# Kernel tuning notes

Measured on AMD Instinct MI355X. Metric: run time of the kernel, lower is better.

The kernel has to match this reference:

```python
import jax, jax.numpy as jnp
import numpy as np

VOCAB = 50257
EMBED_DIM = 768


def setup_inputs() -> dict:
    key = jax.random.key(0)
    k1, k2 = jax.random.split(key)
    x = jax.random.randint(k1, (8, 2048), 0, VOCAB, dtype=jnp.int64 if jax.config.jax_enable_x64 else jnp.int32)
    weight = jax.random.normal(k2, (EMBED_DIM, VOCAB), dtype=jnp.float32)
    return {"x": x, "weight": weight}


def reference(x, weight):
    # Original: one_hot(x, vocab) @ weight.T  ==  gather rows of weight.T
    # weight: [embed_dim, vocab]; output: [batch, seq, embed_dim]
    return jnp.take(weight.T, x, axis=0)
```

## Files before the change

kernel.cpp:

```cpp
#include <hip/hip_runtime.h>


#define VOCAB 50257
#define EMBED 768
#define WINB 32
#define NWIN 1571
#define RG 8
#define ROWS 96
#define LSTRIDE 36
#define CAP 64

__device__ __forceinline__ int xcd_swizzle(int bid, int nwg) {
  const int NX = 8;
  int q = nwg / NX;
  int xcd = bid % NX, idx = bid / NX;
  return xcd * q + idx;
}

__global__ __launch_bounds__(256) void scatter_kernel(const int* __restrict__ x,
                                                      int* __restrict__ cur,
                                                      int* __restrict__ buckets,
                                                      int* __restrict__ spill_cnt,
                                                      int* __restrict__ spill,
                                                      int n) {
  int i = blockIdx.x * blockDim.x + threadIdx.x;
  if (i < n) {
    int v = x[i];
    int win = v >> 5;
    int p = atomicAdd(&cur[win], 1);
    if (p < CAP) {
      buckets[win * CAP + p] = (i << 5) | (v & 31);
    } else {
      int s = atomicAdd(spill_cnt, 1);
      spill[s] = (i << 16) | v;
    }
  }
}

__global__ __launch_bounds__(256) void gather_kernel(const float* __restrict__ w,
                                                     const int* __restrict__ cur,
                                                     const int* __restrict__ buckets,
                                                     const int* __restrict__ spill_cnt,
                                                     const int* __restrict__ spill,
                                                     float* __restrict__ out) {
  __shared__ float lds[ROWS * LSTRIDE];
  __shared__ int toks[CAP];
  const int logical = xcd_swizzle(blockIdx.x, NWIN * RG);
  const int wid = logical % NWIN;
  const int rg  = logical / NWIN;
  const int row0 = rg * ROWS;
  const int col0 = wid * WINB;
  const int tid = threadIdx.x;
  const int wave = tid >> 6, lane = tid & 63;

  int m = cur[wid];
  if (m > CAP) m = CAP;

  if (tid < m) toks[tid] = buckets[wid * CAP + tid];

  if (wid != NWIN - 1) {
    #pragma unroll
    for (int k = 0; k < 3; ++k) {
      int j = k * 256 + tid;
      int r = j >> 3, g = j & 7;
      float4 v = *(const float4*)&w[(size_t)(row0 + r) * VOCAB + col0 + (g << 2)];
      *(float4*)&lds[r * LSTRIDE + (g << 2)] = v;
    }
  } else {
    for (int k = 0; k < 3; ++k) {
      int j = k * 256 + tid;
      int r = j >> 3, g = j & 7;
      float4 v;
      float* pv = (float*)&v;
      for (int u = 0; u < 4; ++u) {
        int c = col0 + (g << 2) + u;
        pv[u] = (c < VOCAB) ? w[(size_t)(row0 + r) * VOCAB + c] : 0.f;
      }
      *(float4*)&lds[r * LSTRIDE + (g << 2)] = v;
    }
  }
  __syncthreads();

  for (int i = wave; i < m; i += 4) {
    int pk = toks[i];
    int t = pk >> 5, c = pk & 31;
    float* o = &out[(size_t)t * EMBED + row0];
    __builtin_nontemporal_store(lds[lane * LSTRIDE + c], &o[lane]);
    if (lane < ROWS - 64)
      __builtin_nontemporal_store(lds[(64 + lane) * LSTRIDE + c], &o[64 + lane]);
  }

  if (blockIdx.x < 64) {
    int cnt = *spill_cnt;
    for (int s = blockIdx.x; s < cnt; s += 64) {
      int pk = spill[s];
      int t = pk >> 16, v = pk & 0xFFFF;
      for (int e = tid; e < EMBED; e += 256)
        out[(size_t)t * EMBED + e] = w[(size_t)e * VOCAB + v];
    }
  }
}

extern "C" void kernel_launch(void* const* d_in, const int* in_sizes, int n_in,
                              void* d_out, int out_size, void* d_ws, size_t ws_size,
                              hipStream_t stream) {
  const int*   x = (const int*)d_in[0];
  const float* w = (const float*)d_in[1];
  float* out = (float*)d_out;
  const int n = in_sizes[0];

  int* cur       = (int*)d_ws;
  int* spill_cnt = cur + NWIN;
  int* spill     = spill_cnt + 1;
  int* buckets   = spill + n;

  hipMemsetAsync(cur, 0, (NWIN + 1) * sizeof(int), stream);
  scatter_kernel<<<(n + 255) / 256, 256, 0, stream>>>(x, cur, buckets,
                                                      spill_cnt, spill, n);
  gather_kernel<<<NWIN * RG, 256, 0, stream>>>(w, cur, buckets,
                                               spill_cnt, spill, out);
}
```

Measured before the change: 46.78 us.

## Make gather kernel persistent with register prefetch of next vocab window

Replaces the one-block-per-(window,row-group) grid of about 12.5k blocks with a persistent grid of 2048 blocks. Each block loops over vocab windows with stride 256 and issues the next window's weight tile and token bucket into registers while it scatters the current one from LDS. The row group is tied to blockIdx&7, which the code intends to map to XCDs. The aim is to cut block launch overhead and hide global load latency behind the output stores, at the cost of fewer blocks in flight, extra barriers per iteration and higher register pressure.

```diff
diff --git a/kernel.cpp b/kernel.cpp
--- a/kernel.cpp
+++ b/kernel.cpp
@@ -5,17 +5,11 @@
 #define EMBED 768
 #define WINB 32
 #define NWIN 1571
-#define RG 8
 #define ROWS 96
 #define LSTRIDE 36
 #define CAP 64
-
-__device__ __forceinline__ int xcd_swizzle(int bid, int nwg) {
-  const int NX = 8;
-  int q = nwg / NX;
-  int xcd = bid % NX, idx = bid / NX;
-  return xcd * q + idx;
-}
+#define NBLK 2048
+#define NPX 256
 
 __global__ __launch_bounds__(256) void scatter_kernel(const int* __restrict__ x,
                                                       int* __restrict__ cur,
@@ -45,58 +39,65 @@
                                                      float* __restrict__ out) {
   __shared__ float lds[ROWS * LSTRIDE];
   __shared__ int toks[CAP];
-  const int logical = xcd_swizzle(blockIdx.x, NWIN * RG);
-  const int wid = logical % NWIN;
-  const int rg  = logical / NWIN;
-  const int row0 = rg * ROWS;
-  const int col0 = wid * WINB;
   const int tid = threadIdx.x;
-  const int wave = tid >> 6, lane = tid & 63;
+  const int b = blockIdx.x;
 
-  int m = cur[wid];
-  if (m > CAP) m = CAP;
-
-  if (tid < m) toks[tid] = buckets[wid * CAP + tid];
-
-  if (wid != NWIN - 1) {
-    #pragma unroll
-    for (int k = 0; k < 3; ++k) {
-      int j = k * 256 + tid;
-      int r = j >> 3, g = j & 7;
-      float4 v = *(const float4*)&w[(size_t)(row0 + r) * VOCAB + col0 + (g << 2)];
-      *(float4*)&lds[r * LSTRIDE + (g << 2)] = v;
-    }
-  } else {
-    for (int k = 0; k < 3; ++k) {
-      int j = k * 256 + tid;
-      int r = j >> 3, g = j & 7;
-      float4 v;
-      float* pv = (float*)&v;
-      for (int u = 0; u < 4; ++u) {
-        int c = col0 + (g << 2) + u;
-        pv[u] = (c < VOCAB) ? w[(size_t)(row0 + r) * VOCAB + c] : 0.f;
-      }
-      *(float4*)&lds[r * LSTRIDE + (g << 2)] = v;
-    }
-  }
-  __syncthreads();
-
-  for (int i = wave; i < m; i += 4) {
-    int pk = toks[i];
-    int t = pk >> 5, c = pk & 31;
-    float* o = &out[(size_t)t * EMBED + row0];
-    __builtin_nontemporal_store(lds[lane * LSTRIDE + c], &o[lane]);
-    if (lane < ROWS - 64)
-      __builtin_nontemporal_store(lds[(64 + lane) * LSTRIDE + c], &o[64 + lane]);
-  }
-
-  if (blockIdx.x < 64) {
+  if (b < 64) {
     int cnt = *spill_cnt;
-    for (int s = blockIdx.x; s < cnt; s += 64) {
+    for (int s = b; s < cnt; s += 64) {
       int pk = spill[s];
       int t = pk >> 16, v = pk & 0xFFFF;
       for (int e = tid; e < EMBED; e += 256)
         out[(size_t)t * EMBED + e] = w[(size_t)e * VOCAB + v];
+    }
+  }
+
+  const int xcd = b & 7, s0 = b >> 3;
+  const int row0 = xcd * ROWS;
+  const int wave = tid >> 6, lane = tid & 63;
+  const int rr = tid >> 3, g4 = (tid & 7) << 2;
+
+  float4 pf0, pf1, pf2;
+  int ptk = 0, pcnt = 0;
+
+  auto issue = [&](int wid) {
+    const float* base = w + (size_t)(row0 + rr) * VOCAB + wid * WINB + g4;
+    if (wid != NWIN - 1) {
+      pf0 = *(const float4*)(base);
+      pf1 = *(const float4*)(base + (size_t)32 * VOCAB);
+      pf2 = *(const float4*)(base + (size_t)64 * VOCAB);
+    } else {
+      float* p0 = (float*)&pf0; float* p1 = (float*)&pf1; float* p2 = (float*)&pf2;
+      for (int u = 0; u < 4; ++u) {
+        bool ok = wid * WINB + g4 + u < VOCAB;
+        p0[u] = ok ? base[u] : 0.f;
+        p1[u] = ok ? base[(size_t)32 * VOCAB + u] : 0.f;
+        p2[u] = ok ? base[(size_t)64 * VOCAB + u] : 0.f;
+      }
+    }
+    if (tid < CAP) ptk = buckets[wid * CAP + tid];
+    pcnt = cur[wid];
+  };
+
+  issue(s0);
+  for (int m = s0; m < NWIN; m += NPX) {
+    __syncthreads();
+    *(float4*)&lds[rr * LSTRIDE + g4] = pf0;
+    *(float4*)&lds[(rr + 32) * LSTRIDE + g4] = pf1;
+    *(float4*)&lds[(rr + 64) * LSTRIDE + g4] = pf2;
+    if (tid < CAP) toks[tid] = ptk;
+    int mcnt = pcnt > CAP ? CAP : pcnt;
+    int mn = m + NPX;
+    if (mn < NWIN) issue(mn);
+    __syncthreads();
+
+    for (int i = wave; i < mcnt; i += 4) {
+      int pk = toks[i];
+      int t = pk >> 5, c = pk & 31;
+      float* o = &out[(size_t)t * EMBED + row0];
+      __builtin_nontemporal_store(lds[lane * LSTRIDE + c], &o[lane]);
+      if (lane < ROWS - 64)
+        __builtin_nontemporal_store(lds[(64 + lane) * LSTRIDE + c], &o[64 + lane]);
     }
   }
 }
@@ -117,6 +118,6 @@
   hipMemsetAsync(cur, 0, (NWIN + 1) * sizeof(int), stream);
   scatter_kernel<<<(n + 255) / 256, 256, 0, stream>>>(x, cur, buckets,
                                                       spill_cnt, spill, n);
-  gather_kernel<<<NWIN * RG, 256, 0, stream>>>(w, cur, buckets,
-                                               spill_cnt, spill, out);
+  gather_kernel<<<NBLK, 256, 0, stream>>>(w, cur, buckets,
+                                          spill_cnt, spill, out);
 }
```

New measurement: 45.95 us. About the same (-1.8%).

## Use smaller row groups with transposed LDS tile and move spill handling first

Applied to the files above, without the earlier changes.

Splits each vocab window into 16 row groups of 48 embedding rows handled by 128-thread blocks instead of 8 groups of 96 with 256 threads. The weight tile is now stored transposed in shared memory, so each token's output row reads one contiguous LDS run, and each wave emits one 48-lane store per token. Spill tokens are processed at block start instead of at the end. This doubles the block count and redundant token-list loads per window, with less LDS per block, trading per-block work for more parallelism and fewer LDS bank conflicts.

```diff
diff --git a/kernel.cpp b/kernel.cpp
--- a/kernel.cpp
+++ b/kernel.cpp
@@ -5,17 +5,10 @@
 #define EMBED 768
 #define WINB 32
 #define NWIN 1571
-#define RG 8
-#define ROWS 96
-#define LSTRIDE 36
+#define RG 16
+#define ROWS 48
+#define RST 50
 #define CAP 64
-
-__device__ __forceinline__ int xcd_swizzle(int bid, int nwg) {
-  const int NX = 8;
-  int q = nwg / NX;
-  int xcd = bid % NX, idx = bid / NX;
-  return xcd * q + idx;
-}
 
 __global__ __launch_bounds__(256) void scatter_kernel(const int* __restrict__ x,
                                                       int* __restrict__ cur,
@@ -37,67 +30,75 @@
   }
 }
 
-__global__ __launch_bounds__(256) void gather_kernel(const float* __restrict__ w,
+__device__ __forceinline__ int xcd_swizzle(int bid, int nwg) {
+  const int NX = 8;
+  int q = nwg / NX;
+  return (bid % NX) * q + bid / NX;
+}
+
+__global__ __launch_bounds__(128) void gather_kernel(const float* __restrict__ w,
                                                      const int* __restrict__ cur,
                                                      const int* __restrict__ buckets,
                                                      const int* __restrict__ spill_cnt,
                                                      const int* __restrict__ spill,
                                                      float* __restrict__ out) {
-  __shared__ float lds[ROWS * LSTRIDE];
+  __shared__ float lds[WINB * RST];
   __shared__ int toks[CAP];
-  const int logical = xcd_swizzle(blockIdx.x, NWIN * RG);
+  const int tid = threadIdx.x;
+  const int b = blockIdx.x;
+
+  if (b < 64) {
+    int cnt = *spill_cnt;
+    for (int s = b; s < cnt; s += 64) {
+      int pk = spill[s];
+      int t = pk >> 16, v = pk & 0xFFFF;
+      for (int e = tid; e < EMBED; e += 128)
+        out[(size_t)t * EMBED + e] = w[(size_t)e * VOCAB + v];
+    }
+  }
+
+  const int logical = xcd_swizzle(b, RG * NWIN);
+  const int rg  = logical / NWIN;
   const int wid = logical % NWIN;
-  const int rg  = logical / NWIN;
   const int row0 = rg * ROWS;
   const int col0 = wid * WINB;
-  const int tid = threadIdx.x;
-  const int wave = tid >> 6, lane = tid & 63;
 
-  int m = cur[wid];
-  if (m > CAP) m = CAP;
-
-  if (tid < m) toks[tid] = buckets[wid * CAP + tid];
+  int pcnt = cur[wid];
+  if (tid < CAP) toks[tid] = buckets[wid * CAP + tid];
 
   if (wid != NWIN - 1) {
     #pragma unroll
     for (int k = 0; k < 3; ++k) {
-      int j = k * 256 + tid;
-      int r = j >> 3, g = j & 7;
-      float4 v = *(const float4*)&w[(size_t)(row0 + r) * VOCAB + col0 + (g << 2)];
-      *(float4*)&lds[r * LSTRIDE + (g << 2)] = v;
+      int j = k * 128 + tid;
+      int r = j >> 3, g4 = (j & 7) << 2;
+      float4 v = *(const float4*)&w[(size_t)(row0 + r) * VOCAB + col0 + g4];
+      lds[(g4 + 0) * RST + r] = v.x;
+      lds[(g4 + 1) * RST + r] = v.y;
+      lds[(g4 + 2) * RST + r] = v.z;
+      lds[(g4 + 3) * RST + r] = v.w;
     }
   } else {
+    #pragma unroll
     for (int k = 0; k < 3; ++k) {
-      int j = k * 256 + tid;
-      int r = j >> 3, g = j & 7;
-      float4 v;
-      float* pv = (float*)&v;
+      int j = k * 128 + tid;
+      int r = j >> 3, g4 = (j & 7) << 2;
       for (int u = 0; u < 4; ++u) {
-        int c = col0 + (g << 2) + u;
-        pv[u] = (c < VOCAB) ? w[(size_t)(row0 + r) * VOCAB + c] : 0.f;
+        int c = col0 + g4 + u;
+        lds[(g4 + u) * RST + r] = (c < VOCAB)
+            ? w[(size_t)(row0 + r) * VOCAB + c] : 0.f;
       }
-      *(float4*)&lds[r * LSTRIDE + (g << 2)] = v;
     }
   }
   __syncthreads();
 
-  for (int i = wave; i < m; i += 4) {
+  int mcnt = pcnt > CAP ? CAP : pcnt;
+  const int wave = tid >> 6, lane = tid & 63;
+  for (int i = wave; i < mcnt; i += 2) {
     int pk = toks[i];
     int t = pk >> 5, c = pk & 31;
-    float* o = &out[(size_t)t * EMBED + row0];
-    __builtin_nontemporal_store(lds[lane * LSTRIDE + c], &o[lane]);
-    if (lane < ROWS - 64)
-      __builtin_nontemporal_store(lds[(64 + lane) * LSTRIDE + c], &o[64 + lane]);
-  }
-
-  if (blockIdx.x < 64) {
-    int cnt = *spill_cnt;
-    for (int s = blockIdx.x; s < cnt; s += 64) {
-      int pk = spill[s];
-      int t = pk >> 16, v = pk & 0xFFFF;
-      for (int e = tid; e < EMBED; e += 256)
-        out[(size_t)t * EMBED + e] = w[(size_t)e * VOCAB + v];
-    }
+    if (lane < ROWS)
+      __builtin_nontemporal_store(lds[c * RST + lane],
+                                  &out[(size_t)t * EMBED + row0 + lane]);
   }
 }
 
@@ -117,6 +118,6 @@
   hipMemsetAsync(cur, 0, (NWIN + 1) * sizeof(int), stream);
   scatter_kernel<<<(n + 255) / 256, 256, 0, stream>>>(x, cur, buckets,
                                                       spill_cnt, spill, n);
-  gather_kernel<<<NWIN * RG, 256, 0, stream>>>(w, cur, buckets,
+  gather_kernel<<<RG * NWIN, 128, 0, stream>>>(w, cur, buckets,
                                                spill_cnt, spill, out);
 }
```

New measurement: 46.15 us. Within noise of the previous version (-1.3%).
